# Performance work log

Hardware: AMD Instinct MI355X
Metric: run time of the kernel (lower is better)

## Reference

```python
import jax, jax.numpy as jnp
import numpy as np

H = 768
I = 3072
E = 8
B, S = 2, 512
EPS = 1e-12


def setup_inputs() -> dict:
    key = jax.random.key(0)
    ks = jax.random.split(key, 8)
    hidden_states = jax.random.normal(ks[0], (B, S, H), dtype=jnp.float32)
    expert_idx = jax.random.randint(ks[1], (B * S,), 0, E)
    scale1 = 1.0 / np.sqrt(H)
    scale2 = 1.0 / np.sqrt(I)
    W1 = jax.random.uniform(ks[2], (E, H, I), jnp.float32, -scale1, scale1)
    b1 = jax.random.uniform(ks[3], (E, I), jnp.float32, -scale1, scale1)
    W2 = jax.random.uniform(ks[4], (E, I, H), jnp.float32, -scale2, scale2)
    b2 = jax.random.uniform(ks[5], (E, H), jnp.float32, -scale2, scale2)
    gamma = jnp.ones((H,), jnp.float32)
    beta = jnp.zeros((H,), jnp.float32)
    return {
        "hidden_states": hidden_states,
        "expert_idx": expert_idx,
        "W1": W1, "b1": b1, "W2": W2, "b2": b2,
        "gamma": gamma, "beta": beta,
    }


def _moe_ln(hidden_states, expert_idx, W1, b1, W2, b2, gamma, beta):
    b, s, h = hidden_states.shape
    x = hidden_states.reshape(-1, h)  # [T, H]
    out = jnp.zeros_like(x)
    # loop over the small fixed expert count; select per-token results by mask
    for e in range(E):
        inter = jax.nn.gelu(x @ W1[e] + b1[e], approximate=False)
        y_e = inter @ W2[e] + b2[e]
        out = jnp.where((expert_idx == e)[:, None], y_e, out)
    y = out.reshape(b, s, h) + hidden_states  # residual
    mu = jnp.mean(y, axis=-1, keepdims=True)
    var = jnp.mean(jnp.square(y - mu), axis=-1, keepdims=True)
    return (y - mu) * jax.lax.rsqrt(var + EPS) * gamma + beta


def reference(hidden_states, expert_idx, W1, b1, W2, b2, gamma, beta):
    return _moe_ln(hidden_states, expert_idx, W1, b1, W2, b2, gamma, beta)
```

## Files before the change

### kernel.cpp

```cpp
#include <hip/hip_runtime.h>
#include <math.h>

#define T_TOK 1024
#define H_DIM 768
#define I_DIM 3072
#define E_NUM 8
#define BM    128
#define BK    64
#define MSLOTS 16
#define KSPLIT2 4

typedef __attribute__((ext_vector_type(8))) short  short8;
typedef __attribute__((ext_vector_type(4))) float  f32x4;
typedef __attribute__((ext_vector_type(4))) int    int4v;

__device__ __forceinline__ unsigned short f2bf(float f) {
  union { float f; unsigned u; } a; a.f = f;
  unsigned r = a.u + 0x7FFFu + ((a.u >> 16) & 1u);
  return (unsigned short)(r >> 16);
}
__device__ __forceinline__ float gelu_exact(float x) {
  return 0.5f * x * (1.0f + erff(x * 0.70710678118654752f));
}
__device__ __forceinline__ int swz(int row, int k) {
  return row * BK + (k ^ ((row & 7) << 3));
}

__global__ __launch_bounds__(1024) void route_kernel(
    const int* __restrict__ eidx, int* __restrict__ perm,
    int* __restrict__ tile_e, int* __restrict__ tile_row,
    int* __restrict__ tile_len, int* __restrict__ ntiles) {
  __shared__ int wcnt[16][E_NUM];
  __shared__ int wpre[16][E_NUM];
  __shared__ int offsh[E_NUM + 1];
  const int t = threadIdx.x;
  const int lane = t & 63, wave = t >> 6;
  const int e = eidx[t];
  unsigned long long myMask = 0;
#pragma unroll
  for (int ee = 0; ee < E_NUM; ++ee) {
    unsigned long long m = __ballot(e == ee);
    if (ee == e) myMask = m;
    if (lane == 0) wcnt[wave][ee] = __popcll(m);
  }
  const int rank = __popcll(myMask & ((1ull << lane) - 1ull));
  __syncthreads();
  if (t < 16 * E_NUM) {
    const int w = t >> 3, ee = t & 7;
    int p = 0;
    for (int w2 = 0; w2 < w; ++w2) p += wcnt[w2][ee];
    wpre[w][ee] = p;
  }
  __syncthreads();
  if (t <= E_NUM) {
    int off = 0;
    for (int ee = 0; ee < t; ++ee) off += wpre[15][ee] + wcnt[15][ee];
    offsh[t] = off;
  }
  __syncthreads();
  perm[offsh[e] + wpre[wave][e] + rank] = t;
  if (t == 0) {
    int n = 0;
    for (int ee = 0; ee < E_NUM; ++ee)
      for (int r = offsh[ee]; r < offsh[ee + 1]; r += BM) {
        tile_e[n] = ee; tile_row[n] = r;
        tile_len[n] = min(offsh[ee + 1] - r, BM); ++n;
      }
    *ntiles = n;
    for (int i = n; i < MSLOTS; ++i) { tile_e[i] = 0; tile_row[i] = 0; tile_len[i] = 0; }
  }
}

__global__ void gather_kernel(const float* __restrict__ x,
                              const int* __restrict__ perm,
                              unsigned short* __restrict__ xg) {
  const int idx = blockIdx.x * 256 + threadIdx.x;
  if (idx >= T_TOK * (H_DIM / 8)) return;
  const int p = idx / (H_DIM / 8);
  const int c = (idx % (H_DIM / 8)) * 8;
  const int t = perm[p];
  const float* src = x + (size_t)t * H_DIM + c;
  const float4 v0 = *(const float4*)(src);
  const float4 v1 = *(const float4*)(src + 4);
  short8 o;
  o[0] = (short)f2bf(v0.x); o[1] = (short)f2bf(v0.y);
  o[2] = (short)f2bf(v0.z); o[3] = (short)f2bf(v0.w);
  o[4] = (short)f2bf(v1.x); o[5] = (short)f2bf(v1.y);
  o[6] = (short)f2bf(v1.z); o[7] = (short)f2bf(v1.w);
  *(short8*)(xg + (size_t)p * H_DIM + c) = o;
}

template <int N_FULL, int K_FULL, int KLOOP, bool IS_FFN1>
__global__ __launch_bounds__(256, 3) void moe_gemm(
    const unsigned short* __restrict__ A,
    const float* __restrict__ W,
    const float* __restrict__ bias,
    const int* __restrict__ tile_e, const int* __restrict__ tile_row,
    const int* __restrict__ tile_len, const int* __restrict__ ntiles,
    unsigned short* __restrict__ out_bf,
    float* __restrict__ part) {
  constexpr int BN = 64;
  constexpr int NF = BN / 32;
  constexpr int KT = KLOOP / BK;

  const int slot = blockIdx.y;
  if (slot >= *ntiles) return;
  const int e    = tile_e[slot];
  const int row0 = tile_row[slot];
  const int len  = tile_len[slot];
  const int n0   = blockIdx.x * BN;
  const int kbase = blockIdx.z * KLOOP;
  const float* We = W + (size_t)e * K_FULL * N_FULL;

  __shared__ unsigned short As[2][BM * BK];
  __shared__ unsigned short Bs[2][BN * BK];

  const int tid  = threadIdx.x;
  const int lane = tid & 63;
  const int wave = tid >> 6;
  const int wr = wave >> 1, wc = wave & 1;
  const int lr = lane & 15;
  const int lk = (lane >> 4) * 8;
  const int bn = tid & 63;
  const int kb = tid >> 6;

  f32x4 acc[4][NF] = {};
  int4v areg0[4], areg1[4];
  float breg0[16], breg1[16];

  auto load_tile = [&](int kt, int4v* ar, float* br) {
    const int k0 = kbase + kt * BK;
#pragma unroll
    for (int i = 0; i < 4; ++i) {
      const int c = tid + i * 256;
      const int r = c >> 3, kc = (c & 7) << 3;
      int grow = row0 + r; grow = grow < T_TOK ? grow : (T_TOK - 1);
      ar[i] = *(const int4v*)(A + (size_t)grow * K_FULL + k0 + kc);
    }
    const float* wp = We + (size_t)(k0 + kb * 16) * N_FULL + n0 + bn;
#pragma unroll
    for (int j = 0; j < 16; ++j)
      br[j] = wp[(size_t)j * N_FULL];
  };
  auto store_lds = [&](int buf, const int4v* ar, const float* br) {
#pragma unroll
    for (int i = 0; i < 4; ++i) {
      const int c = tid + i * 256;
      const int r = c >> 3, kc = (c & 7) << 3;
      *(int4v*)(&As[buf][swz(r, kc)]) = ar[i];
    }
    short8 p0, p1;
#pragma unroll
    for (int j = 0; j < 8; ++j) { p0[j] = (short)f2bf(br[j]); p1[j] = (short)f2bf(br[8 + j]); }
    *(short8*)(&Bs[buf][swz(bn, kb * 16)])     = p0;
    *(short8*)(&Bs[buf][swz(bn, kb * 16 + 8)]) = p1;
  };
  auto mfma_tile = [&](int buf) {
#pragma unroll
    for (int ks = 0; ks < 2; ++ks) {
      const int kk = ks * 32 + lk;
      short8 af[4], bfr[NF];
#pragma unroll
      for (int m = 0; m < 4; ++m)
        af[m] = *(const short8*)(&As[buf][swz(wr * 64 + m * 16 + lr, kk)]);
#pragma unroll
      for (int n = 0; n < NF; ++n)
        bfr[n] = *(const short8*)(&Bs[buf][swz(wc * 32 + n * 16 + lr, kk)]);
#pragma unroll
      for (int m = 0; m < 4; ++m)
#pragma unroll
        for (int n = 0; n < NF; ++n)
          acc[m][n] = __builtin_amdgcn_mfma_f32_16x16x32_bf16(af[m], bfr[n], acc[m][n], 0, 0, 0);
    }
  };

  load_tile(0, areg0, breg0);
  load_tile(1, areg1, breg1);
#pragma unroll 1
  for (int kt = 0; kt < KT; kt += 2) {
    store_lds(0, areg0, breg0);
    if (kt + 2 < KT) load_tile(kt + 2, areg0, breg0);
    asm volatile("s_waitcnt lgkmcnt(0)" ::: "memory");
    __builtin_amdgcn_s_barrier();
    __builtin_amdgcn_sched_barrier(0);
    mfma_tile(0);
    store_lds(1, areg1, breg1);
    if (kt + 3 < KT) load_tile(kt + 3, areg1, breg1);
    asm volatile("s_waitcnt lgkmcnt(0)" ::: "memory");
    __builtin_amdgcn_s_barrier();
    __builtin_amdgcn_sched_barrier(0);
    mfma_tile(1);
  }

#pragma unroll
  for (int n = 0; n < NF; ++n) {
    const int gc = n0 + wc * 32 + n * 16 + lr;
    float bv = 0.f;
    if constexpr (IS_FFN1) bv = bias[(size_t)e * N_FULL + gc];
#pragma unroll
    for (int m = 0; m < 4; ++m) {
      const int rbase = wr * 64 + m * 16 + (lane >> 4) * 4;
#pragma unroll
      for (int j = 0; j < 4; ++j) {
        const int rl = rbase + j;
        if (rl < len) {
          if constexpr (IS_FFN1) {
            out_bf[(size_t)(row0 + rl) * N_FULL + gc] = f2bf(gelu_exact(acc[m][n][j] + bv));
          } else {
            part[((size_t)blockIdx.z * T_TOK + row0 + rl) * N_FULL + gc] = acc[m][n][j];
          }
        }
      }
    }
  }
}

__global__ void ln_kernel(const float* __restrict__ part,
                          const float* __restrict__ x,
                          const int* __restrict__ perm,
                          const int* __restrict__ eidx,
                          const float* __restrict__ b2,
                          const float* __restrict__ gamma,
                          const float* __restrict__ beta,
                          float* __restrict__ out) {
  const int p = blockIdx.x;
  const int tid = threadIdx.x;
  const int t = perm[p];
  const int e = eidx[t];
  float v[3], s = 0.f, ss = 0.f;
#pragma unroll
  for (int i = 0; i < 3; ++i) {
    const int c = tid + i * 256;
    float a = x[(size_t)t * H_DIM + c] + b2[(size_t)e * H_DIM + c];
#pragma unroll
    for (int s4 = 0; s4 < KSPLIT2; ++s4)
      a += part[((size_t)s4 * T_TOK + p) * H_DIM + c];
    v[i] = a; s += a; ss += a * a;
  }
#pragma unroll
  for (int o = 32; o; o >>= 1) { s += __shfl_down(s, o); ss += __shfl_down(ss, o); }
  __shared__ float ps[4], pss[4];
  __shared__ float mu_s, ir_s;
  const int w = tid >> 6;
  if ((tid & 63) == 0) { ps[w] = s; pss[w] = ss; }
  __syncthreads();
  if (tid == 0) {
    const float S = ps[0] + ps[1] + ps[2] + ps[3];
    const float SS = pss[0] + pss[1] + pss[2] + pss[3];
    const float mu = S * (1.0f / H_DIM);
    const float var = SS * (1.0f / H_DIM) - mu * mu;
    mu_s = mu; ir_s = rsqrtf(var + 1e-12f);
  }
  __syncthreads();
  const float mu = mu_s, ir = ir_s;
#pragma unroll
  for (int i = 0; i < 3; ++i) {
    const int c = tid + i * 256;
    out[(size_t)t * H_DIM + c] = (v[i] - mu) * ir * gamma[c] + beta[c];
  }
}

extern "C" void kernel_launch(void* const* d_in, const int* in_sizes, int n_in,
                              void* d_out, int out_size, void* d_ws, size_t ws_size,
                              hipStream_t stream) {
  const float* x     = (const float*)d_in[0];
  const int*   eidx  = (const int*)d_in[1];
  const float* W1    = (const float*)d_in[2];
  const float* b1    = (const float*)d_in[3];
  const float* W2    = (const float*)d_in[4];
  const float* b2    = (const float*)d_in[5];
  const float* gamma = (const float*)d_in[6];
  const float* beta  = (const float*)d_in[7];
  float* out = (float*)d_out;

  char* ws = (char*)d_ws;
  int* perm     = (int*)(ws);
  int* tile_e   = (int*)(ws + 4096);
  int* tile_row = (int*)(ws + 4352);
  int* tile_len = (int*)(ws + 4608);
  int* ntiles   = (int*)(ws + 4864);
  unsigned short* xg    = (unsigned short*)(ws + 8192);
  unsigned short* inter = xg + (size_t)T_TOK * H_DIM;
  float* part = (float*)(ws + 8192 + 2 * (size_t)T_TOK * (H_DIM + I_DIM));

  route_kernel<<<1, T_TOK, 0, stream>>>(eidx, perm, tile_e, tile_row, tile_len, ntiles);
  gather_kernel<<<(T_TOK * (H_DIM / 8) + 255) / 256, 256, 0, stream>>>(x, perm, xg);
  moe_gemm<I_DIM, H_DIM, H_DIM, true><<<dim3(I_DIM / 64, MSLOTS, 1), 256, 0, stream>>>(
      xg, W1, b1, tile_e, tile_row, tile_len, ntiles, inter, nullptr);
  moe_gemm<H_DIM, I_DIM, I_DIM / KSPLIT2, false><<<dim3(H_DIM / 64, MSLOTS, KSPLIT2), 256, 0, stream>>>(
      inter, W2, nullptr, tile_e, tile_row, tile_len, ntiles, nullptr, part);
  ln_kernel<<<T_TOK, 256, 0, stream>>>(part, x, perm, eidx, b2, gamma, beta, out);
  (void)in_sizes; (void)n_in; (void)out_size; (void)ws_size;
}
```

Baseline: 77.11 us.

## Load MFMA operands straight from global memory, dropping LDS staging and barriers

The grouped GEMM no longer stages A and B tiles through shared memory. Each wave loads its MFMA fragments directly from global memory into registers, double-buffered across k-steps, and converts the fp32 weights to bf16 just before the MFMA. This removes the LDS stores and loads, the swizzle and the block barriers, and the occupancy hint in launch bounds is dropped. In exchange, operands that waves used to share are now fetched redundantly from global memory, the weight reads become strided per lane with poor coalescing, and register pressure rises (64 floats plus 16 short8 buffers per thread).

```diff
diff --git a/kernel.cpp b/kernel.cpp
--- a/kernel.cpp
+++ b/kernel.cpp
@@ -12,7 +12,6 @@
 
 typedef __attribute__((ext_vector_type(8))) short  short8;
 typedef __attribute__((ext_vector_type(4))) float  f32x4;
-typedef __attribute__((ext_vector_type(4))) int    int4v;
 
 __device__ __forceinline__ unsigned short f2bf(float f) {
   union { float f; unsigned u; } a; a.f = f;
@@ -21,9 +20,6 @@
 }
 __device__ __forceinline__ float gelu_exact(float x) {
   return 0.5f * x * (1.0f + erff(x * 0.70710678118654752f));
-}
-__device__ __forceinline__ int swz(int row, int k) {
-  return row * BK + (k ^ ((row & 7) << 3));
 }
 
 __global__ __launch_bounds__(1024) void route_kernel(
@@ -91,7 +87,7 @@
 }
 
 template <int N_FULL, int K_FULL, int KLOOP, bool IS_FFN1>
-__global__ __launch_bounds__(256, 3) void moe_gemm(
+__global__ __launch_bounds__(256) void moe_gemm(
     const unsigned short* __restrict__ A,
     const float* __restrict__ W,
     const float* __restrict__ bias,
@@ -99,8 +95,6 @@
     const int* __restrict__ tile_len, const int* __restrict__ ntiles,
     unsigned short* __restrict__ out_bf,
     float* __restrict__ part) {
-  constexpr int BN = 64;
-  constexpr int NF = BN / 32;
   constexpr int KT = KLOOP / BK;
 
   const int slot = blockIdx.y;
@@ -108,92 +102,68 @@
   const int e    = tile_e[slot];
   const int row0 = tile_row[slot];
   const int len  = tile_len[slot];
-  const int n0   = blockIdx.x * BN;
+  const int n0   = blockIdx.x * 64;
   const int kbase = blockIdx.z * KLOOP;
   const float* We = W + (size_t)e * K_FULL * N_FULL;
 
-  __shared__ unsigned short As[2][BM * BK];
-  __shared__ unsigned short Bs[2][BN * BK];
-
-  const int tid  = threadIdx.x;
-  const int lane = tid & 63;
-  const int wave = tid >> 6;
+  const int lane = threadIdx.x & 63;
+  const int wave = threadIdx.x >> 6;
   const int wr = wave >> 1, wc = wave & 1;
-  const int lr = lane & 15;
-  const int lk = (lane >> 4) * 8;
-  const int bn = tid & 63;
-  const int kb = tid >> 6;
-
-  f32x4 acc[4][NF] = {};
-  int4v areg0[4], areg1[4];
-  float breg0[16], breg1[16];
-
-  auto load_tile = [&](int kt, int4v* ar, float* br) {
-    const int k0 = kbase + kt * BK;
-#pragma unroll
-    for (int i = 0; i < 4; ++i) {
-      const int c = tid + i * 256;
-      const int r = c >> 3, kc = (c & 7) << 3;
-      int grow = row0 + r; grow = grow < T_TOK ? grow : (T_TOK - 1);
-      ar[i] = *(const int4v*)(A + (size_t)grow * K_FULL + k0 + kc);
-    }
-    const float* wp = We + (size_t)(k0 + kb * 16) * N_FULL + n0 + bn;
-#pragma unroll
-    for (int j = 0; j < 16; ++j)
-      br[j] = wp[(size_t)j * N_FULL];
-  };
-  auto store_lds = [&](int buf, const int4v* ar, const float* br) {
-#pragma unroll
-    for (int i = 0; i < 4; ++i) {
-      const int c = tid + i * 256;
-      const int r = c >> 3, kc = (c & 7) << 3;
-      *(int4v*)(&As[buf][swz(r, kc)]) = ar[i];
-    }
-    short8 p0, p1;
-#pragma unroll
-    for (int j = 0; j < 8; ++j) { p0[j] = (short)f2bf(br[j]); p1[j] = (short)f2bf(br[8 + j]); }
-    *(short8*)(&Bs[buf][swz(bn, kb * 16)])     = p0;
-    *(short8*)(&Bs[buf][swz(bn, kb * 16 + 8)]) = p1;
-  };
-  auto mfma_tile = [&](int buf) {
-#pragma unroll
-    for (int ks = 0; ks < 2; ++ks) {
-      const int kk = ks * 32 + lk;
-      short8 af[4], bfr[NF];
-#pragma unroll
-      for (int m = 0; m < 4; ++m)
-        af[m] = *(const short8*)(&As[buf][swz(wr * 64 + m * 16 + lr, kk)]);
-#pragma unroll
-      for (int n = 0; n < NF; ++n)
-        bfr[n] = *(const short8*)(&Bs[buf][swz(wc * 32 + n * 16 + lr, kk)]);
-#pragma unroll
-      for (int m = 0; m < 4; ++m)
-#pragma unroll
-        for (int n = 0; n < NF; ++n)
-          acc[m][n] = __builtin_amdgcn_mfma_f32_16x16x32_bf16(af[m], bfr[n], acc[m][n], 0, 0, 0);
-    }
-  };
-
-  load_tile(0, areg0, breg0);
-  load_tile(1, areg1, breg1);
+  const int lr  = lane & 15;
+  const int lkb = (lane >> 4) << 3;
+
+  const unsigned short* aptr[4];
+#pragma unroll
+  for (int m = 0; m < 4; ++m) {
+    int row = row0 + wr * 64 + m * 16 + lr;
+    row = row < T_TOK ? row : (T_TOK - 1);
+    aptr[m] = A + (size_t)row * K_FULL + kbase + lkb;
+  }
+  const float* bp = We + (size_t)(kbase + lkb) * N_FULL + (n0 + wc * 32 + lr);
+
+  f32x4 acc[4][2] = {};
+  short8 a0[8], a1[8];
+  float  b0[32], b1[32];
+
+#define LOAD_A(kt, dst)                                                   \
+  _Pragma("unroll") for (int m = 0; m < 4; ++m)                           \
+  _Pragma("unroll") for (int ks = 0; ks < 2; ++ks)                        \
+    dst[m * 2 + ks] = *(const short8*)(aptr[m] + (kt) * BK + ks * 32);
+#define LOAD_B(kt, dst)                                                   \
+  _Pragma("unroll") for (int ks = 0; ks < 2; ++ks)                        \
+  _Pragma("unroll") for (int n = 0; n < 2; ++n)                           \
+  _Pragma("unroll") for (int j = 0; j < 8; ++j)                           \
+    dst[(ks * 2 + n) * 8 + j] =                                           \
+        bp[(size_t)((kt) * BK + ks * 32 + j) * N_FULL + n * 16];
+#define MFMA_STEP(asrc, bsrc)                                             \
+  _Pragma("unroll") for (int ks = 0; ks < 2; ++ks) {                      \
+    short8 bfr[2];                                                        \
+    _Pragma("unroll") for (int n = 0; n < 2; ++n)                         \
+    _Pragma("unroll") for (int j = 0; j < 8; ++j)                         \
+      bfr[n][j] = (short)f2bf(bsrc[(ks * 2 + n) * 8 + j]);                \
+    _Pragma("unroll") for (int m = 0; m < 4; ++m)                         \
+    _Pragma("unroll") for (int n = 0; n < 2; ++n)                         \
+      acc[m][n] = __builtin_amdgcn_mfma_f32_16x16x32_bf16(                \
+          asrc[m * 2 + ks], bfr[n], acc[m][n], 0, 0, 0);                  \
+  }
+
+  LOAD_A(0, a0) LOAD_B(0, b0)
+  LOAD_A(1, a1) LOAD_B(1, b1)
 #pragma unroll 1
-  for (int kt = 0; kt < KT; kt += 2) {
-    store_lds(0, areg0, breg0);
-    if (kt + 2 < KT) load_tile(kt + 2, areg0, breg0);
-    asm volatile("s_waitcnt lgkmcnt(0)" ::: "memory");
-    __builtin_amdgcn_s_barrier();
-    __builtin_amdgcn_sched_barrier(0);
-    mfma_tile(0);
-    store_lds(1, areg1, breg1);
-    if (kt + 3 < KT) load_tile(kt + 3, areg1, breg1);
-    asm volatile("s_waitcnt lgkmcnt(0)" ::: "memory");
-    __builtin_amdgcn_s_barrier();
-    __builtin_amdgcn_sched_barrier(0);
-    mfma_tile(1);
-  }
-
-#pragma unroll
-  for (int n = 0; n < NF; ++n) {
+  for (int kt = 0; kt < KT - 2; kt += 2) {
+    MFMA_STEP(a0, b0)
+    LOAD_A(kt + 2, a0) LOAD_B(kt + 2, b0)
+    MFMA_STEP(a1, b1)
+    LOAD_A(kt + 3, a1) LOAD_B(kt + 3, b1)
+  }
+  MFMA_STEP(a0, b0)
+  MFMA_STEP(a1, b1)
+#undef LOAD_A
+#undef LOAD_B
+#undef MFMA_STEP
+
+#pragma unroll
+  for (int n = 0; n < 2; ++n) {
     const int gc = n0 + wc * 32 + n * 16 + lr;
     float bv = 0.f;
     if constexpr (IS_FFN1) bv = bias[(size_t)e * N_FULL + gc];
```

After: 118.8 us. 1.54x slower.
